# Optimization experiments

Hardware: AMD Instinct MI355X
Metric: run time of the kernel (lower is better)

## Reference

```python
import jax, jax.numpy as jnp
import numpy as np

V = 100000      # item vocab
N1, N2, N3 = 100000, 20000, 5000
EMB = 128       # embedding_dim == hidden_dim
H, Dh = 8, 16   # num_heads, per-head dim (H*Dh == EMB)
NEG_SLOPE = 0.2


def setup_inputs() -> dict:
    key = jax.random.key(0)
    ks = jax.random.split(key, 32)
    ki = iter(range(32))
    def nrm(shape, scale=0.1):
        return jax.random.normal(ks[next(ki)], shape, dtype=jnp.float32) * scale
    def ridx(n, hi):
        return jax.random.randint(ks[next(ki)], (n,), 0, hi, dtype=jnp.int32)
    inp = {}
    # graph structure
    inp['item_ids'] = ridx(N1, V)
    inp['seq1_src'] = ridx(600000, N1); inp['seq1_dst'] = ridx(600000, N1)
    inp['seq2_src'] = ridx(120000, N2); inp['seq2_dst'] = ridx(120000, N2)
    inp['seq3_src'] = ridx(30000, N3);  inp['seq3_dst'] = ridx(30000, N3)
    inp['up1_src']   = ridx(200000, N1); inp['up1_dst']   = ridx(200000, N2)
    inp['down1_src'] = ridx(200000, N2); inp['down1_dst'] = ridx(200000, N1)
    inp['up2_src']   = ridx(60000, N2);  inp['up2_dst']   = ridx(60000, N3)
    inp['down2_src'] = ridx(60000, N3);  inp['down2_dst'] = ridx(60000, N2)
    # parameters: 7 GATConvs in order [seq1, seq2, seq3, up1, down1, up2, down2]
    inp['item_emb'] = nrm((V, EMB), 1.0)
    inp['fc_w']   = nrm((7, EMB, H * Dh))   # DGL fc (bias=False)
    inp['attn_l'] = nrm((7, H, Dh))
    inp['attn_r'] = nrm((7, H, Dh))
    inp['conv_b'] = nrm((7, H * Dh))        # GATConv bias
    # 3 readout MLPs: Linear(hid,hid)->ReLU->Linear(hid,emb)
    inp['r_w1'] = nrm((3, EMB, EMB)); inp['r_b1'] = nrm((3, EMB))
    inp['r_w2'] = nrm((3, EMB, EMB)); inp['r_b2'] = nrm((3, EMB))
    inp['gran_w'] = jnp.ones((3,), dtype=jnp.float32)
    return inp


def gat(h_src, h_dst, src, dst, W, al, ar, b, residual):
    """DGL GATConv (eval mode, no dropout, no activation)."""
    Ns, Nd = h_src.shape[0], h_dst.shape[0]
    fs = (h_src @ W).reshape(Ns, H, Dh)   # [Ns,H,Dh]
    fd = (h_dst @ W).reshape(Nd, H, Dh)
    el = jnp.sum(fs * al, axis=-1)        # [Ns,H]
    er = jnp.sum(fd * ar, axis=-1)        # [Nd,H]
    e = jax.nn.leaky_relu(el[src] + er[dst], NEG_SLOPE)   # [E,H]
    m = jax.ops.segment_max(e, dst, num_segments=Nd)      # edge-softmax per dst
    ez = jnp.exp(e - m[dst])
    denom = jax.ops.segment_sum(ez, dst, num_segments=Nd)
    alpha = ez / denom[dst]                                # [E,H]
    msg = alpha[:, :, None] * fs[src]                      # [E,H,Dh]
    out = jax.ops.segment_sum(msg, dst, num_segments=Nd)   # [Nd,H,Dh]
    if residual:  # in_feats == H*Dh -> identity residual
        out = out + h_dst.reshape(Nd, H, Dh)
    out = out + b.reshape(1, H, Dh)
    return out.reshape(Nd, H * Dh)


def reference(item_emb, fc_w, attn_l, attn_r, conv_b,
              r_w1, r_b1, r_w2, r_b2, gran_w,
              item_ids, seq1_src, seq1_dst, seq2_src, seq2_dst,
              seq3_src, seq3_dst, up1_src, up1_dst, down1_src, down1_dst,
              up2_src, up2_dst, down2_src, down2_dst):
    h1 = item_emb[item_ids]                           # gran_1 from embedding lookup
    h2 = jnp.zeros((N2, EMB), dtype=item_emb.dtype)   # gran_2/3 init to zeros
    h3 = jnp.zeros((N3, EMB), dtype=item_emb.dtype)
    def g(i, hs, hd, s, d, res):
        return gat(hs, hd, s, d, fc_w[i], attn_l[i], attn_r[i], conv_b[i], res)
    out1 = g(0, h1, h1, seq1_src, seq1_dst, True) + g(4, h2, h1, down1_src, down1_dst, False)
    out2 = (g(1, h2, h2, seq2_src, seq2_dst, True)
            + g(3, h1, h2, up1_src, up1_dst, False)
            + g(6, h3, h2, down2_src, down2_dst, False))
    out3 = g(2, h3, h3, seq3_src, seq3_dst, True) + g(5, h2, h3, up2_src, up2_dst, False)
    reprs = []
    for k, x in enumerate((out1, out2, out3)):
        r = jax.nn.relu(x @ r_w1[k] + r_b1[k]) @ r_w2[k] + r_b2[k]
        reprs.append(jnp.mean(r, axis=0))             # session readout mean
    stack = jnp.stack(reprs, axis=0)                  # [3, EMB]
    weights = jax.nn.softmax(gran_w)
    fused = jnp.sum(stack * weights[:, None], axis=0) # [EMB]
    return fused, stack, weights
```

## Files before the change

kernel.cpp:

```cpp
#include <hip/hip_runtime.h>
#include <math.h>

#define N1 100000
#define N2 20000
#define EMB 128
#define NH 8
#define TILE 64
#define LPAD 132

static constexpr float NEG = 0.2f;

#define F4C(v, c) ((c) == 0 ? (v).x : (c) == 1 ? (v).y : (c) == 2 ? (v).z : (v).w)

__global__ __launch_bounds__(256) void k_feat64(
    const float* __restrict__ item_emb, const int* __restrict__ item_ids,
    const float* __restrict__ fc_w, const float* __restrict__ attn_l,
    const float* __restrict__ attn_r,
    float* __restrict__ fs0, float* __restrict__ fs3,
    float* __restrict__ el0, float* __restrict__ er0, float* __restrict__ el3)
{
    __shared__ float xs[TILE][LPAD];

    const int tid = threadIdx.x;
    const int nbase = blockIdx.x * TILE;

    #pragma unroll
    for (int r = 0; r < 8; ++r) {
        int f4 = r * 256 + tid;
        int t  = f4 >> 5;
        int c4 = f4 & 31;
        int node = nbase + t;
        if (node < N1) {
            int row = item_ids[node];
            ((float4*)&xs[t][0])[c4] =
                ((const float4*)(item_emb + (size_t)row * EMB))[c4];
        }
    }
    __syncthreads();

    const int cg = tid & 31;
    const int rg = tid >> 5;
    const int j0 = cg * 4;
    const float* W0 = fc_w + j0;
    const float* W3 = fc_w + 3 * EMB * EMB + j0;

    float a0[8][4], a3[8][4];
    #pragma unroll
    for (int r = 0; r < 8; ++r)
        #pragma unroll
        for (int c = 0; c < 4; ++c) { a0[r][c] = 0.f; a3[r][c] = 0.f; }

    float4 wc0[4], wc3[4], wn0[4], wn3[4];
    #pragma unroll
    for (int kk = 0; kk < 4; ++kk) {
        wc0[kk] = *((const float4*)(W0 + (size_t)kk * EMB));
        wc3[kk] = *((const float4*)(W3 + (size_t)kk * EMB));
    }

    for (int k = 0; k < EMB; k += 4) {
        const int kn = k + 4;
        if (kn < EMB) {
            #pragma unroll
            for (int kk = 0; kk < 4; ++kk) {
                wn0[kk] = *((const float4*)(W0 + (size_t)(kn + kk) * EMB));
                wn3[kk] = *((const float4*)(W3 + (size_t)(kn + kk) * EMB));
            }
        }
        #pragma unroll
        for (int r = 0; r < 8; ++r) {
            float4 x = *((const float4*)&xs[rg * 8 + r][k]);
            #pragma unroll
            for (int c = 0; c < 4; ++c) {
                float acc0 = a0[r][c], acc3 = a3[r][c];
                acc0 = fmaf(x.x, F4C(wc0[0], c), acc0);
                acc0 = fmaf(x.y, F4C(wc0[1], c), acc0);
                acc0 = fmaf(x.z, F4C(wc0[2], c), acc0);
                acc0 = fmaf(x.w, F4C(wc0[3], c), acc0);
                acc3 = fmaf(x.x, F4C(wc3[0], c), acc3);
                acc3 = fmaf(x.y, F4C(wc3[1], c), acc3);
                acc3 = fmaf(x.z, F4C(wc3[2], c), acc3);
                acc3 = fmaf(x.w, F4C(wc3[3], c), acc3);
                a0[r][c] = acc0; a3[r][c] = acc3;
            }
        }
        if (kn < EMB) {
            #pragma unroll
            for (int kk = 0; kk < 4; ++kk) { wc0[kk] = wn0[kk]; wc3[kk] = wn3[kk]; }
        }
    }

    #pragma unroll
    for (int r = 0; r < 8; ++r) {
        int row = nbase + rg * 8 + r;
        if (row < N1) {
            float4 v0 = make_float4(a0[r][0], a0[r][1], a0[r][2], a0[r][3]);
            float4 v3 = make_float4(a3[r][0], a3[r][1], a3[r][2], a3[r][3]);
            *((float4*)(fs0 + (size_t)row * EMB + j0)) = v0;
            *((float4*)(fs3 + (size_t)row * EMB + j0)) = v3;
        }
    }

    float al0v[4], ar0v[4], al3v[4];
    #pragma unroll
    for (int c = 0; c < 4; ++c) {
        al0v[c] = attn_l[j0 + c];
        ar0v[c] = attn_r[j0 + c];
        al3v[c] = attn_l[3 * EMB + j0 + c];
    }
    const int head = j0 >> 4;
    #pragma unroll
    for (int r = 0; r < 8; ++r) {
        float pe = a0[r][0]*al0v[0] + a0[r][1]*al0v[1] + a0[r][2]*al0v[2] + a0[r][3]*al0v[3];
        float pr = a0[r][0]*ar0v[0] + a0[r][1]*ar0v[1] + a0[r][2]*ar0v[2] + a0[r][3]*ar0v[3];
        float p3 = a3[r][0]*al3v[0] + a3[r][1]*al3v[1] + a3[r][2]*al3v[2] + a3[r][3]*al3v[3];
        pe += __shfl_xor(pe, 1); pe += __shfl_xor(pe, 2);
        pr += __shfl_xor(pr, 1); pr += __shfl_xor(pr, 2);
        p3 += __shfl_xor(p3, 1); p3 += __shfl_xor(p3, 2);
        int row = nbase + rg * 8 + r;
        if ((cg & 3) == 0 && row < N1) {
            el0[(size_t)row * NH + head] = pe;
            er0[(size_t)row * NH + head] = pr;
            el3[(size_t)row * NH + head] = p3;
        }
    }
}

__global__ __launch_bounds__(256) void k_count2(
    const int* __restrict__ s1d, int nE1,
    const int* __restrict__ u1d, int nE3, int* __restrict__ cnt)
{
    int i = blockIdx.x * 256 + threadIdx.x;
    if (i < nE1) atomicAdd(&cnt[s1d[i]], 1);
    else if (i < nE1 + nE3) atomicAdd(&cnt[N1 + u1d[i - nE1]], 1);
}

__global__ __launch_bounds__(256) void k_scan_partial(
    const int* __restrict__ cnt, int n, int* __restrict__ part)
{
    __shared__ int sh[256];
    int base = blockIdx.x * 1024 + threadIdx.x * 4;
    int s = 0;
    #pragma unroll
    for (int k = 0; k < 4; ++k) { int i = base + k; if (i < n) s += cnt[i]; }
    sh[threadIdx.x] = s;
    __syncthreads();
    for (int off = 128; off > 0; off >>= 1) {
        if (threadIdx.x < off) sh[threadIdx.x] += sh[threadIdx.x + off];
        __syncthreads();
    }
    if (threadIdx.x == 0) part[blockIdx.x] = sh[0];
}

__global__ __launch_bounds__(256) void k_scan_mid(int* part, int np)
{
    __shared__ int sh[256];
    int tid = threadIdx.x;
    int v = (tid < np) ? part[tid] : 0;
    sh[tid] = v;
    __syncthreads();
    for (int off = 1; off < 256; off <<= 1) {
        int t = (tid >= off) ? sh[tid - off] : 0;
        __syncthreads();
        sh[tid] += t;
        __syncthreads();
    }
    if (tid < np) part[tid] = sh[tid] - v;
}

__global__ __launch_bounds__(256) void k_scan_final(
    const int* __restrict__ cnt, const int* __restrict__ part, int n, int nE,
    int* __restrict__ off, int* __restrict__ cur)
{
    __shared__ int sh[256];
    int tid = threadIdx.x;
    int base = blockIdx.x * 1024 + tid * 4;
    int c[4]; int s = 0;
    #pragma unroll
    for (int k = 0; k < 4; ++k) { int i = base + k; c[k] = (i < n) ? cnt[i] : 0; s += c[k]; }
    sh[tid] = s;
    __syncthreads();
    int own = s;
    for (int offv = 1; offv < 256; offv <<= 1) {
        int t = (tid >= offv) ? sh[tid - offv] : 0;
        __syncthreads();
        sh[tid] += t;
        __syncthreads();
    }
    int excl = sh[tid] - own + part[blockIdx.x];
    #pragma unroll
    for (int k = 0; k < 4; ++k) {
        int i = base + k;
        if (i < n) { off[i] = excl; cur[i] = excl; excl += c[k]; }
    }
    if (blockIdx.x == 0 && tid == 0) off[n] = nE;
}

__global__ __launch_bounds__(256) void k_scatter2(
    const int* __restrict__ s1s, const int* __restrict__ s1d, int nE1,
    const int* __restrict__ u1s, const int* __restrict__ u1d, int nE3,
    int* __restrict__ cur, int* __restrict__ esrc)
{
    int i = blockIdx.x * 256 + threadIdx.x;
    if (i < nE1) {
        int pos = atomicAdd(&cur[s1d[i]], 1);
        esrc[pos] = s1s[i];
    } else if (i < nE1 + nE3) {
        int j = i - nE1;
        int pos = atomicAdd(&cur[N1 + u1d[j]], 1);
        esrc[pos] = u1s[j];
    }
}

__global__ __launch_bounds__(256) void k_agg(
    const int* __restrict__ off, const int* __restrict__ esrc,
    const float* __restrict__ el0, const float* __restrict__ er0,
    const float* __restrict__ fs0,
    const float* __restrict__ el3, const float* __restrict__ fs3,
    const float* __restrict__ item_emb, const int* __restrict__ item_ids,
    const float* __restrict__ conv_b,
    float* __restrict__ val1, float* __restrict__ val2)
{
    const int wid  = blockIdx.x * 4 + (threadIdx.x >> 6);
    const int lane = threadIdx.x & 63;
    const int h = lane >> 3;
    const int c = lane * 2;

    const float* el; const float* fs;
    float erh, b0, b1;
    bool g1 = (wid < N1);
    if (g1) {
        el = el0; fs = fs0;
        erh = er0[(size_t)wid * NH + h];
        b0 = conv_b[0 * EMB + c]     + conv_b[4 * EMB + c];
        b1 = conv_b[0 * EMB + c + 1] + conv_b[4 * EMB + c + 1];
    } else {
        el = el3; fs = fs3;
        erh = 0.f;
        b0 = conv_b[3 * EMB + c]     + conv_b[1 * EMB + c]     + conv_b[6 * EMB + c];
        b1 = conv_b[3 * EMB + c + 1] + conv_b[1 * EMB + c + 1] + conv_b[6 * EMB + c + 1];
    }

    const int beg = off[wid], end = off[wid + 1];
    float ax = 0.f, ay = 0.f, wsum = 0.f;
    for (int base = beg; base < end; base += 64) {
        int myS = (base + lane < end) ? esrc[base + lane] : 0;
        int cnt = min(64, end - base);
        int i = 0;
        for (; i + 1 < cnt; i += 2) {
            int sA = __shfl(myS, i);
            int sB = __shfl(myS, i + 1);
            float eA = el[(size_t)sA * NH + h] + erh;
            float eB = el[(size_t)sB * NH + h] + erh;
            eA = (eA > 0.f) ? eA : NEG * eA;
            eB = (eB > 0.f) ? eB : NEG * eB;
            float wA = __expf(eA);
            float wB = __expf(eB);
            float2 fA = ((const float2*)(fs + (size_t)sA * EMB))[lane];
            float2 fB = ((const float2*)(fs + (size_t)sB * EMB))[lane];
            ax = fmaf(wA, fA.x, fmaf(wB, fB.x, ax));
            ay = fmaf(wA, fA.y, fmaf(wB, fB.y, ay));
            wsum += wA + wB;
        }
        if (i < cnt) {
            int s = __shfl(myS, i);
            float e = el[(size_t)s * NH + h] + erh;
            e = (e > 0.f) ? e : NEG * e;
            float w = __expf(e);
            float2 f2 = ((const float2*)(fs + (size_t)s * EMB))[lane];
            ax = fmaf(w, f2.x, ax);
            ay = fmaf(w, f2.y, ay);
            wsum += w;
        }
    }

    float vx = 0.f, vy = 0.f;
    if (end > beg) { float inv = 1.f / wsum; vx = ax * inv; vy = ay * inv; }
    if (g1) {
        float2 r = ((const float2*)(item_emb + (size_t)item_ids[wid] * EMB))[lane];
        vx += r.x; vy += r.y;
    }
    float2 o; o.x = vx + b0; o.y = vy + b1;
    float* out = g1 ? (val1 + (size_t)wid * EMB) : (val2 + (size_t)(wid - N1) * EMB);
    ((float2*)out)[lane] = o;
}

__global__ __launch_bounds__(256) void k_mlp64(
    const float* __restrict__ val, int nrows,
    const float* __restrict__ rw1, const float* __restrict__ rb1,
    float* __restrict__ mean)
{
    __shared__ float xs[TILE][LPAD];
    __shared__ float red[8][EMB];

    const int tid = threadIdx.x;
    const int nbase = blockIdx.x * TILE;

    #pragma unroll
    for (int r = 0; r < 8; ++r) {
        int f4 = r * 256 + tid;
        int t  = f4 >> 5;
        int c4 = f4 & 31;
        int row = nbase + t;
        if (row < nrows)
            ((float4*)&xs[t][0])[c4] =
                ((const float4*)(val + (size_t)row * EMB))[c4];
    }
    __syncthreads();

    const int cg = tid & 31;
    const int rg = tid >> 5;
    const int j0 = cg * 4;
    const float* W = rw1 + j0;

    float a[8][4];
    #pragma unroll
    for (int r = 0; r < 8; ++r)
        #pragma unroll
        for (int c = 0; c < 4; ++c) a[r][c] = 0.f;

    float4 wc[4], wn[4];
    #pragma unroll
    for (int kk = 0; kk < 4; ++kk) wc[kk] = *((const float4*)(W + (size_t)kk * EMB));

    for (int k = 0; k < EMB; k += 4) {
        const int kn = k + 4;
        if (kn < EMB) {
            #pragma unroll
            for (int kk = 0; kk < 4; ++kk)
                wn[kk] = *((const float4*)(W + (size_t)(kn + kk) * EMB));
        }
        #pragma unroll
        for (int r = 0; r < 8; ++r) {
            float4 x = *((const float4*)&xs[rg * 8 + r][k]);
            #pragma unroll
            for (int c = 0; c < 4; ++c) {
                float acc = a[r][c];
                acc = fmaf(x.x, F4C(wc[0], c), acc);
                acc = fmaf(x.y, F4C(wc[1], c), acc);
                acc = fmaf(x.z, F4C(wc[2], c), acc);
                acc = fmaf(x.w, F4C(wc[3], c), acc);
                a[r][c] = acc;
            }
        }
        if (kn < EMB) {
            #pragma unroll
            for (int kk = 0; kk < 4; ++kk) wc[kk] = wn[kk];
        }
    }

    float b1v[4];
    #pragma unroll
    for (int c = 0; c < 4; ++c) b1v[c] = rb1[j0 + c];
    float cs[4] = {0.f, 0.f, 0.f, 0.f};
    #pragma unroll
    for (int r = 0; r < 8; ++r) {
        int row = nbase + rg * 8 + r;
        if (row < nrows) {
            #pragma unroll
            for (int c = 0; c < 4; ++c)
                cs[c] += fmaxf(a[r][c] + b1v[c], 0.f);
        }
    }
    *((float4*)&red[rg][j0]) = make_float4(cs[0], cs[1], cs[2], cs[3]);
    __syncthreads();
    if (tid < EMB) {
        float s = 0.f;
        #pragma unroll
        for (int g = 0; g < 8; ++g) s += red[g][tid];
        atomicAdd(mean + tid, s);
    }
}

__global__ __launch_bounds__(128) void k_final(
    const float* __restrict__ mean1, const float* __restrict__ mean2,
    const float* __restrict__ conv_b,
    const float* __restrict__ r_w1, const float* __restrict__ r_b1,
    const float* __restrict__ r_w2, const float* __restrict__ r_b2,
    const float* __restrict__ gran_w, float* __restrict__ out)
{
    __shared__ float m1[EMB], m2[EMB], x3[EMB], t3[EMB];
    const int j = threadIdx.x;
    m1[j] = mean1[j] * (1.f / N1);
    m2[j] = mean2[j] * (1.f / N2);
    x3[j] = conv_b[2 * EMB + j] + conv_b[5 * EMB + j];
    __syncthreads();

    float a = r_b1[2 * EMB + j];
    for (int k = 0; k < EMB; ++k)
        a = fmaf(x3[k], r_w1[2 * EMB * EMB + k * EMB + j], a);
    t3[j] = fmaxf(a, 0.f);
    __syncthreads();

    float r1 = r_b2[0 * EMB + j];
    float r2 = r_b2[1 * EMB + j];
    float r3 = r_b2[2 * EMB + j];
    for (int k = 0; k < EMB; ++k) {
        r1 = fmaf(m1[k], r_w2[0 * EMB * EMB + k * EMB + j], r1);
        r2 = fmaf(m2[k], r_w2[1 * EMB * EMB + k * EMB + j], r2);
        r3 = fmaf(t3[k], r_w2[2 * EMB * EMB + k * EMB + j], r3);
    }

    float g0 = gran_w[0], g1 = gran_w[1], g2 = gran_w[2];
    float mx = fmaxf(g0, fmaxf(g1, g2));
    float e0 = expf(g0 - mx), e1 = expf(g1 - mx), e2 = expf(g2 - mx);
    float s = e0 + e1 + e2;
    float w0 = e0 / s, w1 = e1 / s, w2 = e2 / s;

    out[j]       = w0 * r1 + w1 * r2 + w2 * r3;
    out[128 + j] = r1;
    out[256 + j] = r2;
    out[384 + j] = r3;
    if (j < 3) out[512 + j] = (j == 0) ? w0 : (j == 1) ? w1 : w2;
}

extern "C" void kernel_launch(void* const* d_in, const int* in_sizes, int n_in,
                              void* d_out, int out_size, void* d_ws, size_t ws_size,
                              hipStream_t stream) {
    const int*   item_ids = (const int*)d_in[0];
    const int*   s1s = (const int*)d_in[1];
    const int*   s1d = (const int*)d_in[2];
    const int*   u1s = (const int*)d_in[7];
    const int*   u1d = (const int*)d_in[8];
    const float* item_emb = (const float*)d_in[15];
    const float* fc_w   = (const float*)d_in[16];
    const float* attn_l = (const float*)d_in[17];
    const float* attn_r = (const float*)d_in[18];
    const float* conv_b = (const float*)d_in[19];
    const float* r_w1 = (const float*)d_in[20];
    const float* r_b1 = (const float*)d_in[21];
    const float* r_w2 = (const float*)d_in[22];
    const float* r_b2 = (const float*)d_in[23];
    const float* gran_w = (const float*)d_in[24];

    const int nE1 = in_sizes[1];
    const int nE3 = in_sizes[7];
    const int nEt = nE1 + nE3;
    const int ND  = N1 + N2;

    float* ws = (float*)d_ws;
    float* mean1 = ws;
    float* mean2 = mean1 + EMB;
    int*   cnt   = (int*)(mean2 + EMB);
    size_t zeroN = 2 * EMB + ND;
    int*   off   = cnt + ND;
    int*   cur   = off + ND + 4;
    int*   part  = cur + ND;
    int*   esrc  = part + 128;
    float* fs0   = (float*)(esrc + nEt);
    float* fs3   = fs0 + (size_t)N1 * EMB;
    float* el0   = fs3 + (size_t)N1 * EMB;
    float* er0   = el0 + (size_t)N1 * NH;
    float* el3   = er0 + (size_t)N1 * NH;
    float* val1  = el3 + (size_t)N1 * NH;
    float* val2  = val1 + (size_t)N1 * EMB;

    hipMemsetAsync(ws, 0, zeroN * sizeof(float), stream);

    k_feat64<<<(N1 + TILE - 1) / TILE, 256, 0, stream>>>(
        item_emb, item_ids, fc_w, attn_l, attn_r, fs0, fs3, el0, er0, el3);

    const int nch = (ND + 1023) / 1024;
    k_count2<<<(nEt + 255) / 256, 256, 0, stream>>>(s1d, nE1, u1d, nE3, cnt);
    k_scan_partial<<<nch, 256, 0, stream>>>(cnt, ND, part);
    k_scan_mid<<<1, 256, 0, stream>>>(part, nch);
    k_scan_final<<<nch, 256, 0, stream>>>(cnt, part, ND, nEt, off, cur);
    k_scatter2<<<(nEt + 255) / 256, 256, 0, stream>>>(s1s, s1d, nE1,
                                                      u1s, u1d, nE3, cur, esrc);

    k_agg<<<ND / 4, 256, 0, stream>>>(off, esrc, el0, er0, fs0, el3, fs3,
                                      item_emb, item_ids, conv_b, val1, val2);

    k_mlp64<<<(N1 + TILE - 1) / TILE, 256, 0, stream>>>(
        val1, N1, r_w1 + 0 * EMB * EMB, r_b1 + 0 * EMB, mean1);
    k_mlp64<<<(N2 + TILE - 1) / TILE, 256, 0, stream>>>(
        val2, N2, r_w1 + 1 * EMB * EMB, r_b1 + 1 * EMB, mean2);

    k_final<<<1, 128, 0, stream>>>(mean1, mean2, conv_b, r_w1, r_b1, r_w2, r_b2,
                                   gran_w, (float*)d_out);
}
```

Baseline: 560.4 us.

## Halve node tile to 32, merge two MLP launches, unroll aggregation by four

The feature-transform and readout-MLP kernels now process 32 nodes per block instead of 64, with fewer accumulators per thread, which lowers register pressure and doubles the block count. Bounds checks are dropped because N1 and N2 divide evenly by 32. The two per-granularity MLP launches are merged into one grid that picks its inputs from the block index, saving a launch and a tail. The edge aggregation loop issues four gathers per iteration instead of two to expose more memory-level parallelism. The trade-offs are less weight reuse per block and more registers in the aggregation loop.

```diff
diff --git a/kernel.cpp b/kernel.cpp
--- a/kernel.cpp
+++ b/kernel.cpp
@@ -5,14 +5,16 @@
 #define N2 20000
 #define EMB 128
 #define NH 8
-#define TILE 64
+#define TILE 32
 #define LPAD 132
+#define NB1 (N1 / TILE)
+#define NB2 (N2 / TILE)
 
 static constexpr float NEG = 0.2f;
 
 #define F4C(v, c) ((c) == 0 ? (v).x : (c) == 1 ? (v).y : (c) == 2 ? (v).z : (v).w)
 
-__global__ __launch_bounds__(256) void k_feat64(
+__global__ __launch_bounds__(256) void k_feat32(
     const float* __restrict__ item_emb, const int* __restrict__ item_ids,
     const float* __restrict__ fc_w, const float* __restrict__ attn_l,
     const float* __restrict__ attn_r,
@@ -25,16 +27,13 @@
     const int nbase = blockIdx.x * TILE;
 
     #pragma unroll
-    for (int r = 0; r < 8; ++r) {
+    for (int r = 0; r < 4; ++r) {
         int f4 = r * 256 + tid;
         int t  = f4 >> 5;
         int c4 = f4 & 31;
-        int node = nbase + t;
-        if (node < N1) {
-            int row = item_ids[node];
-            ((float4*)&xs[t][0])[c4] =
-                ((const float4*)(item_emb + (size_t)row * EMB))[c4];
-        }
+        int row = item_ids[nbase + t];
+        ((float4*)&xs[t][0])[c4] =
+            ((const float4*)(item_emb + (size_t)row * EMB))[c4];
     }
     __syncthreads();
 
@@ -44,9 +43,9 @@
     const float* W0 = fc_w + j0;
     const float* W3 = fc_w + 3 * EMB * EMB + j0;
 
-    float a0[8][4], a3[8][4];
-    #pragma unroll
-    for (int r = 0; r < 8; ++r)
+    float a0[4][4], a3[4][4];
+    #pragma unroll
+    for (int r = 0; r < 4; ++r)
         #pragma unroll
         for (int c = 0; c < 4; ++c) { a0[r][c] = 0.f; a3[r][c] = 0.f; }
 
@@ -67,8 +66,8 @@
             }
         }
         #pragma unroll
-        for (int r = 0; r < 8; ++r) {
-            float4 x = *((const float4*)&xs[rg * 8 + r][k]);
+        for (int r = 0; r < 4; ++r) {
+            float4 x = *((const float4*)&xs[rg * 4 + r][k]);
             #pragma unroll
             for (int c = 0; c < 4; ++c) {
                 float acc0 = a0[r][c], acc3 = a3[r][c];
@@ -90,14 +89,12 @@
     }
 
     #pragma unroll
-    for (int r = 0; r < 8; ++r) {
-        int row = nbase + rg * 8 + r;
-        if (row < N1) {
-            float4 v0 = make_float4(a0[r][0], a0[r][1], a0[r][2], a0[r][3]);
-            float4 v3 = make_float4(a3[r][0], a3[r][1], a3[r][2], a3[r][3]);
-            *((float4*)(fs0 + (size_t)row * EMB + j0)) = v0;
-            *((float4*)(fs3 + (size_t)row * EMB + j0)) = v3;
-        }
+    for (int r = 0; r < 4; ++r) {
+        int row = nbase + rg * 4 + r;
+        float4 v0 = make_float4(a0[r][0], a0[r][1], a0[r][2], a0[r][3]);
+        float4 v3 = make_float4(a3[r][0], a3[r][1], a3[r][2], a3[r][3]);
+        *((float4*)(fs0 + (size_t)row * EMB + j0)) = v0;
+        *((float4*)(fs3 + (size_t)row * EMB + j0)) = v3;
     }
 
     float al0v[4], ar0v[4], al3v[4];
@@ -109,15 +106,15 @@
     }
     const int head = j0 >> 4;
     #pragma unroll
-    for (int r = 0; r < 8; ++r) {
+    for (int r = 0; r < 4; ++r) {
         float pe = a0[r][0]*al0v[0] + a0[r][1]*al0v[1] + a0[r][2]*al0v[2] + a0[r][3]*al0v[3];
         float pr = a0[r][0]*ar0v[0] + a0[r][1]*ar0v[1] + a0[r][2]*ar0v[2] + a0[r][3]*ar0v[3];
         float p3 = a3[r][0]*al3v[0] + a3[r][1]*al3v[1] + a3[r][2]*al3v[2] + a3[r][3]*al3v[3];
         pe += __shfl_xor(pe, 1); pe += __shfl_xor(pe, 2);
         pr += __shfl_xor(pr, 1); pr += __shfl_xor(pr, 2);
         p3 += __shfl_xor(p3, 1); p3 += __shfl_xor(p3, 2);
-        int row = nbase + rg * 8 + r;
-        if ((cg & 3) == 0 && row < N1) {
+        int row = nbase + rg * 4 + r;
+        if ((cg & 3) == 0) {
             el0[(size_t)row * NH + head] = pe;
             er0[(size_t)row * NH + head] = pr;
             el3[(size_t)row * NH + head] = p3;
@@ -246,22 +243,30 @@
         int myS = (base + lane < end) ? esrc[base + lane] : 0;
         int cnt = min(64, end - base);
         int i = 0;
-        for (; i + 1 < cnt; i += 2) {
+        for (; i + 3 < cnt; i += 4) {
             int sA = __shfl(myS, i);
             int sB = __shfl(myS, i + 1);
+            int sC = __shfl(myS, i + 2);
+            int sD = __shfl(myS, i + 3);
             float eA = el[(size_t)sA * NH + h] + erh;
             float eB = el[(size_t)sB * NH + h] + erh;
+            float eC = el[(size_t)sC * NH + h] + erh;
+            float eD = el[(size_t)sD * NH + h] + erh;
+            float2 fA = ((const float2*)(fs + (size_t)sA * EMB))[lane];
+            float2 fB = ((const float2*)(fs + (size_t)sB * EMB))[lane];
+            float2 fC = ((const float2*)(fs + (size_t)sC * EMB))[lane];
+            float2 fD = ((const float2*)(fs + (size_t)sD * EMB))[lane];
             eA = (eA > 0.f) ? eA : NEG * eA;
             eB = (eB > 0.f) ? eB : NEG * eB;
-            float wA = __expf(eA);
-            float wB = __expf(eB);
-            float2 fA = ((const float2*)(fs + (size_t)sA * EMB))[lane];
-            float2 fB = ((const float2*)(fs + (size_t)sB * EMB))[lane];
-            ax = fmaf(wA, fA.x, fmaf(wB, fB.x, ax));
-            ay = fmaf(wA, fA.y, fmaf(wB, fB.y, ay));
-            wsum += wA + wB;
-        }
-        if (i < cnt) {
+            eC = (eC > 0.f) ? eC : NEG * eC;
+            eD = (eD > 0.f) ? eD : NEG * eD;
+            float wA = __expf(eA), wB = __expf(eB);
+            float wC = __expf(eC), wD = __expf(eD);
+            ax = fmaf(wA, fA.x, fmaf(wB, fB.x, fmaf(wC, fC.x, fmaf(wD, fD.x, ax))));
+            ay = fmaf(wA, fA.y, fmaf(wB, fB.y, fmaf(wC, fC.y, fmaf(wD, fD.y, ay))));
+            wsum += (wA + wB) + (wC + wD);
+        }
+        for (; i < cnt; ++i) {
             int s = __shfl(myS, i);
             float e = el[(size_t)s * NH + h] + erh;
             e = (e > 0.f) ? e : NEG * e;
@@ -284,26 +289,30 @@
     ((float2*)out)[lane] = o;
 }
 
-__global__ __launch_bounds__(256) void k_mlp64(
-    const float* __restrict__ val, int nrows,
-    const float* __restrict__ rw1, const float* __restrict__ rb1,
-    float* __restrict__ mean)
+__global__ __launch_bounds__(256) void k_mlp32(
+    const float* __restrict__ val1, const float* __restrict__ val2,
+    const float* __restrict__ r_w1, const float* __restrict__ r_b1,
+    float* __restrict__ mean1, float* __restrict__ mean2)
 {
     __shared__ float xs[TILE][LPAD];
     __shared__ float red[8][EMB];
 
     const int tid = threadIdx.x;
-    const int nbase = blockIdx.x * TILE;
-
-    #pragma unroll
-    for (int r = 0; r < 8; ++r) {
+    const int b = blockIdx.x;
+    const bool g1 = (b < NB1);
+    const float* val  = g1 ? val1 : val2;
+    const float* rw1  = g1 ? r_w1 : r_w1 + EMB * EMB;
+    const float* rb1  = g1 ? r_b1 : r_b1 + EMB;
+    float*       mean = g1 ? mean1 : mean2;
+    const int nbase = (g1 ? b : b - NB1) * TILE;
+
+    #pragma unroll
+    for (int r = 0; r < 4; ++r) {
         int f4 = r * 256 + tid;
         int t  = f4 >> 5;
         int c4 = f4 & 31;
-        int row = nbase + t;
-        if (row < nrows)
-            ((float4*)&xs[t][0])[c4] =
-                ((const float4*)(val + (size_t)row * EMB))[c4];
+        ((float4*)&xs[t][0])[c4] =
+            ((const float4*)(val + (size_t)(nbase + t) * EMB))[c4];
     }
     __syncthreads();
 
@@ -312,9 +321,9 @@
     const int j0 = cg * 4;
     const float* W = rw1 + j0;
 
-    float a[8][4];
-    #pragma unroll
-    for (int r = 0; r < 8; ++r)
+    float a[4][4];
+    #pragma unroll
+    for (int r = 0; r < 4; ++r)
         #pragma unroll
         for (int c = 0; c < 4; ++c) a[r][c] = 0.f;
 
@@ -330,8 +339,8 @@
                 wn[kk] = *((const float4*)(W + (size_t)(kn + kk) * EMB));
         }
         #pragma unroll
-        for (int r = 0; r < 8; ++r) {
-            float4 x = *((const float4*)&xs[rg * 8 + r][k]);
+        for (int r = 0; r < 4; ++r) {
+            float4 x = *((const float4*)&xs[rg * 4 + r][k]);
             #pragma unroll
             for (int c = 0; c < 4; ++c) {
                 float acc = a[r][c];
@@ -353,14 +362,10 @@
     for (int c = 0; c < 4; ++c) b1v[c] = rb1[j0 + c];
     float cs[4] = {0.f, 0.f, 0.f, 0.f};
     #pragma unroll
-    for (int r = 0; r < 8; ++r) {
-        int row = nbase + rg * 8 + r;
-        if (row < nrows) {
-            #pragma unroll
-            for (int c = 0; c < 4; ++c)
-                cs[c] += fmaxf(a[r][c] + b1v[c], 0.f);
-        }
-    }
+    for (int r = 0; r < 4; ++r)
+        #pragma unroll
+        for (int c = 0; c < 4; ++c)
+            cs[c] += fmaxf(a[r][c] + b1v[c], 0.f);
     *((float4*)&red[rg][j0]) = make_float4(cs[0], cs[1], cs[2], cs[3]);
     __syncthreads();
     if (tid < EMB) {
@@ -456,7 +461,7 @@
 
     hipMemsetAsync(ws, 0, zeroN * sizeof(float), stream);
 
-    k_feat64<<<(N1 + TILE - 1) / TILE, 256, 0, stream>>>(
+    k_feat32<<<NB1, 256, 0, stream>>>(
         item_emb, item_ids, fc_w, attn_l, attn_r, fs0, fs3, el0, er0, el3);
 
     const int nch = (ND + 1023) / 1024;
@@ -470,10 +475,7 @@
     k_agg<<<ND / 4, 256, 0, stream>>>(off, esrc, el0, er0, fs0, el3, fs3,
                                       item_emb, item_ids, conv_b, val1, val2);
 
-    k_mlp64<<<(N1 + TILE - 1) / TILE, 256, 0, stream>>>(
-        val1, N1, r_w1 + 0 * EMB * EMB, r_b1 + 0 * EMB, mean1);
-    k_mlp64<<<(N2 + TILE - 1) / TILE, 256, 0, stream>>>(
-        val2, N2, r_w1 + 1 * EMB * EMB, r_b1 + 1 * EMB, mean2);
+    k_mlp32<<<NB1 + NB2, 256, 0, stream>>>(val1, val2, r_w1, r_b1, mean1, mean2);
 
     k_final<<<1, 128, 0, stream>>>(mean1, mean2, conv_b, r_w1, r_b1, r_w2, r_b2,
                                    gran_w, (float*)d_out);
```

Result: no change. 567.8 us (+1.3%).
